# Performance work log

Measured on AMD Instinct MI355X. Metric: run time of the kernel, lower is better.

## Reference

```python
import jax, jax.numpy as jnp
import numpy as np

N = 20000      # nodes per snapshot
E = 160000     # edges per snapshot
T = 8          # timesteps
F_IN = 256     # nfeat
HEADS = 4      # GAT heads
C = 128        # nhid_graph (per-head GAT out, concat=False -> mean)
GH = 128       # nhid_gru
NC = 2         # nclass
NEG_SLOPE = 0.2


def setup_inputs() -> dict:
    key = jax.random.key(0)
    ks = jax.random.split(key, 16)
    s = 0.05
    return {
        "graph": jax.random.randint(ks[0], (T, 2, E), 0, N),
        "fts": jax.random.normal(ks[1], (T, N, F_IN), dtype=jnp.float32),
        "time_steps": T,
        # GATConv params (PyG-style): lin weight, att_src/att_dst, bias
        "W_gat": jax.random.normal(ks[2], (F_IN, HEADS * C), dtype=jnp.float32) * s,
        "att_src": jax.random.normal(ks[3], (HEADS, C), dtype=jnp.float32) * s,
        "att_dst": jax.random.normal(ks[4], (HEADS, C), dtype=jnp.float32) * s,
        "b_gat": jax.random.normal(ks[5], (C,), dtype=jnp.float32) * s,
        # GRU params (torch layout: [3H, in], gates order r,z,n)
        "W_ih": jax.random.normal(ks[6], (3 * GH, C), dtype=jnp.float32) * s,
        "W_hh": jax.random.normal(ks[7], (3 * GH, GH), dtype=jnp.float32) * s,
        "b_ih": jax.random.normal(ks[8], (3 * GH,), dtype=jnp.float32) * s,
        "b_hh": jax.random.normal(ks[9], (3 * GH,), dtype=jnp.float32) * s,
        # Attention ('general'): linear_in [H,H] no bias, linear_out [H,2H] no bias
        "W_att_in": jax.random.normal(ks[10], (GH, GH), dtype=jnp.float32) * s,
        "W_att_out": jax.random.normal(ks[11], (GH, 2 * GH), dtype=jnp.float32) * s,
        # final classifier
        "W_cls": jax.random.normal(ks[12], (NC, GH), dtype=jnp.float32) * s,
        "b_cls": jax.random.normal(ks[13], (NC,), dtype=jnp.float32) * s,
    }


def _segment_softmax(logits, seg, num_segments):
    # logits: [E', H], seg: [E'] destination node ids
    m = jax.ops.segment_max(logits, seg, num_segments=num_segments)
    m = jnp.where(jnp.isfinite(m), m, 0.0)
    e = jnp.exp(logits - m[seg])
    s = jax.ops.segment_sum(e, seg, num_segments=num_segments)
    return e / (s[seg] + 1e-16)


def _gat_step(x, edge_index, W_gat, att_src, att_dst, b_gat):
    # PyG GATConv: concat=False (mean over heads), negative_slope=0.2,
    # add_self_loops=True; eval mode so attention dropout is identity.
    n = x.shape[0]
    xw = (x @ W_gat).reshape(n, HEADS, C)                 # [N,H,C]
    loops = jnp.arange(n, dtype=edge_index.dtype)
    src = jnp.concatenate([edge_index[0], loops])         # [E']
    dst = jnp.concatenate([edge_index[1], loops])
    a_src = jnp.einsum('nhc,hc->nh', xw, att_src)         # [N,H]
    a_dst = jnp.einsum('nhc,hc->nh', xw, att_dst)
    alpha = jax.nn.leaky_relu(a_src[src] + a_dst[dst], NEG_SLOPE)  # [E',H]
    alpha = _segment_softmax(alpha, dst, n)
    msg = xw[src] * alpha[..., None]                      # [E',H,C]
    out = jax.ops.segment_sum(msg, dst, num_segments=n)   # [N,H,C]
    return out.mean(axis=1) + b_gat                       # [N,C]


def _gru(y, W_ih, W_hh, b_ih, b_hh):
    # y: [T, N, C]; torch GRU equations, h0 = 0
    n = y.shape[1]
    def step(h, x):
        gi = x @ W_ih.T + b_ih
        gh = h @ W_hh.T + b_hh
        i_r, i_z, i_n = jnp.split(gi, 3, axis=-1)
        h_r, h_z, h_n = jnp.split(gh, 3, axis=-1)
        r = jax.nn.sigmoid(i_r + h_r)
        z = jax.nn.sigmoid(i_z + h_z)
        nn_ = jnp.tanh(i_n + r * h_n)
        h_new = (1.0 - z) * nn_ + z * h
        return h_new, h_new
    h0 = jnp.zeros((n, GH), dtype=y.dtype)
    last, full = jax.lax.scan(step, h0, y)
    return full, last  # [T,N,GH], [N,GH]


def reference(graph, fts, time_steps, W_gat, att_src, att_dst, b_gat,
              W_ih, W_hh, b_ih, b_hh, W_att_in, W_att_out, W_cls, b_cls):
    # per-timestep GAT + leaky_relu(0.2)
    ys = [jax.nn.leaky_relu(
            _gat_step(fts[i], graph[i], W_gat, att_src, att_dst, b_gat),
            NEG_SLOPE)
          for i in range(time_steps)]
    y = jnp.stack(ys)                                     # [T,N,C]
    context, last = _gru(y, W_ih, W_hh, b_ih, b_hh)
    query = last[:, None, :]                              # [N,1,GH]
    context = jnp.transpose(context, (1, 0, 2))           # [N,T,GH]
    # Attention('general')
    q = query @ W_att_in.T                                # [N,1,GH]
    scores = jnp.einsum('nod,ntd->not', q, context)       # [N,1,T]
    w = jax.nn.softmax(scores, axis=-1)
    mix = jnp.einsum('not,ntd->nod', w, context)          # [N,1,GH]
    combined = jnp.concatenate([mix, q], axis=-1)         # [N,1,2GH]
    att_out = jnp.tanh(combined @ W_att_out.T)            # [N,1,GH]
    output = jax.nn.leaky_relu(att_out.reshape(-1, GH), NEG_SLOPE)
    logits = output @ W_cls.T + b_cls                     # [N,NC]
    return jax.nn.log_softmax(logits, axis=1)
```

## Files before the change

kernel.cpp:

```cpp
#include <hip/hip_runtime.h>
#include <hip/hip_bf16.h>
#include <math.h>

#define N_NODES 20000
#define N_EDGES 160000
#define T_STEPS 8
#define F_INC   256
#define HEADS   4
#define CCH     128
#define KC      512
#define GHD     128
#define G3      384
#define SLOPE   0.2f
#define SEG     (N_EDGES + N_NODES)

typedef unsigned short u16;
typedef __attribute__((ext_vector_type(8))) short bf16x8;
typedef __attribute__((ext_vector_type(4))) float f32x4;

__device__ __forceinline__ float leakyf(float x) { return x > 0.f ? x : SLOPE * x; }
__device__ __forceinline__ float b2f(u16 u) {
  union { unsigned int i; float f; } x; x.i = ((unsigned int)u) << 16; return x.f;
}
__device__ __forceinline__ u16 f2b(float f) {
  union { float f; unsigned int i; } u; u.f = f;
  unsigned int r = u.i + 0x7FFFu + ((u.i >> 16) & 1u);
  return (u16)(r >> 16);
}
__device__ __forceinline__ float sigf(float x) { return 1.f / (1.f + expf(-x)); }

__device__ __forceinline__ void gload16(const void* g, void* l) {
  __builtin_amdgcn_global_load_lds(
      (const __attribute__((address_space(1))) unsigned int*)g,
      (__attribute__((address_space(3))) unsigned int*)l, 16, 0, 0);
}

template <int OBF, int FUSE>
__global__ __launch_bounds__(256) void gemm_bf16(
    const u16* __restrict__ A, const u16* __restrict__ B,
    const float* __restrict__ bias, void* __restrict__ Cout,
    int M, int K, int Nt, int swz,
    const float* __restrict__ attS, const float* __restrict__ attD,
    float* __restrict__ asrc, float* __restrict__ adst)
{
  __shared__ u16 As[128][32];
  __shared__ u16 Bs[128][32];
  __shared__ float s_as[128], s_ad[128];
  const int tid  = threadIdx.x;
  const int wave = tid >> 6, lane = tid & 63;
  const int wr = (wave >> 1) * 64, wc = (wave & 1) * 64;
  int bx = blockIdx.x, by = blockIdx.y;
  if (swz) {
    const int gx = gridDim.x;
    const int nwg = gx * (int)gridDim.y;
    const int lin = by * gx + bx;
    const int q = nwg >> 3, r = nwg & 7;
    const int xcd = lin & 7, idx = lin >> 3;
    const int wg = (xcd < r ? xcd * (q + 1) : r * (q + 1) + (xcd - r) * q) + idx;
    bx = wg % gx; by = wg / gx;
  }
  const int bm = by * 128, bn = bx * 128;
  const int l15 = lane & 15, g = lane >> 4;

  if (FUSE && tid < 128) { s_as[tid] = 0.f; s_ad[tid] = 0.f; }

  const int sr = tid >> 2, sd = tid & 3;
  const int ss = sd ^ ((sr >> 1) & 3);
  const u16* aS0 = A + (size_t)min(bm + sr,      M - 1) * K + ss * 8;
  const u16* aS1 = A + (size_t)min(bm + 64 + sr, M - 1) * K + ss * 8;
  const u16* bS0 = B + (size_t)(bn + sr)      * K + ss * 8;
  const u16* bS1 = B + (size_t)(bn + 64 + sr) * K + ss * 8;
  u16* lA0 = &As[0][0] + (size_t)(tid & ~63) * 8;
  u16* lA1 = lA0 + 2048;
  u16* lB0 = &Bs[0][0] + (size_t)(tid & ~63) * 8;
  u16* lB1 = lB0 + 2048;

  f32x4 acc[4][4];
  #pragma unroll
  for (int m = 0; m < 4; ++m)
    #pragma unroll
    for (int n = 0; n < 4; ++n)
      #pragma unroll
      for (int j = 0; j < 4; ++j) acc[m][n][j] = 0.f;

  const int nK = K >> 5;
  for (int kt = 0; kt < nK; ++kt) {
    const int ko = kt * 32;
    gload16(aS0 + ko, lA0);
    gload16(aS1 + ko, lA1);
    gload16(bS0 + ko, lB0);
    gload16(bS1 + ko, lB1);
    __syncthreads();
    bf16x8 af[4], bfr[4];
    #pragma unroll
    for (int m = 0; m < 4; ++m) {
      int row = wr + m * 16 + l15;
      af[m] = *(const bf16x8*)&As[row][(g ^ ((row >> 1) & 3)) * 8];
      int rowb = wc + m * 16 + l15;
      bfr[m] = *(const bf16x8*)&Bs[rowb][(g ^ ((rowb >> 1) & 3)) * 8];
    }
    #pragma unroll
    for (int m = 0; m < 4; ++m)
      #pragma unroll
      for (int n = 0; n < 4; ++n)
        acc[m][n] = __builtin_amdgcn_mfma_f32_16x16x32_bf16(af[m], bfr[n], acc[m][n], 0, 0, 0);
    __syncthreads();
  }
  #pragma unroll
  for (int m = 0; m < 4; ++m) {
    int row0 = bm + wr + m * 16 + g * 4;
    #pragma unroll
    for (int n = 0; n < 4; ++n) {
      int col = bn + wc + n * 16 + l15;
      float bv = bias ? bias[col] : 0.f;
      #pragma unroll
      for (int j = 0; j < 4; ++j) {
        int row = row0 + j;
        if (row < M) {
          float v = acc[m][n][j] + bv;
          if (OBF) ((u16*)Cout)[(size_t)row * Nt + col] = f2b(v);
          else     ((float*)Cout)[(size_t)row * Nt + col] = v;
        }
      }
    }
  }
  if (FUSE) {
    float ps[4][4], pd[4][4];
    #pragma unroll
    for (int m = 0; m < 4; ++m)
      #pragma unroll
      for (int j = 0; j < 4; ++j) { ps[m][j] = 0.f; pd[m][j] = 0.f; }
    #pragma unroll
    for (int n = 0; n < 4; ++n) {
      int cl = wc + n * 16 + l15;
      float wsv = attS[bn + cl], wdv = attD[bn + cl];
      #pragma unroll
      for (int m = 0; m < 4; ++m)
        #pragma unroll
        for (int j = 0; j < 4; ++j) {
          ps[m][j] = fmaf(acc[m][n][j], wsv, ps[m][j]);
          pd[m][j] = fmaf(acc[m][n][j], wdv, pd[m][j]);
        }
    }
    #pragma unroll
    for (int m = 0; m < 4; ++m)
      #pragma unroll
      for (int j = 0; j < 4; ++j)
        #pragma unroll
        for (int msk = 8; msk >= 1; msk >>= 1) {
          ps[m][j] += __shfl_xor(ps[m][j], msk);
          pd[m][j] += __shfl_xor(pd[m][j], msk);
        }
    if (l15 == 0) {
      #pragma unroll
      for (int m = 0; m < 4; ++m)
        #pragma unroll
        for (int j = 0; j < 4; ++j) {
          atomicAdd(&s_as[wr + m * 16 + g * 4 + j], ps[m][j]);
          atomicAdd(&s_ad[wr + m * 16 + g * 4 + j], pd[m][j]);
        }
    }
    __syncthreads();
    if (tid < 128) {
      int row = bm + tid;
      if (row < M) {
        int h = bn >> 7;
        asrc[(size_t)row * 4 + h] = s_as[tid];
        adst[(size_t)row * 4 + h] = s_ad[tid];
      }
    }
  }
}

__global__ void convert_f32_bf16(const float* __restrict__ src, u16* __restrict__ dst, int n) {
  int i = (blockIdx.x * 256 + threadIdx.x) * 8;
  if (i >= n) return;
  float4 v0 = *(const float4*)(src + i);
  float4 v1 = *(const float4*)(src + i + 4);
  bf16x8 o;
  o[0] = (short)f2b(v0.x); o[1] = (short)f2b(v0.y);
  o[2] = (short)f2b(v0.z); o[3] = (short)f2b(v0.w);
  o[4] = (short)f2b(v1.x); o[5] = (short)f2b(v1.y);
  o[6] = (short)f2b(v1.z); o[7] = (short)f2b(v1.w);
  *(bf16x8*)(dst + i) = o;
}

__global__ void convert_weights(const float* __restrict__ w_ih, const float* __restrict__ w_hh,
                                const float* __restrict__ w_in, const float* __restrict__ w_out,
                                u16* __restrict__ wihb, u16* __restrict__ whhb,
                                u16* __restrict__ winb, u16* __restrict__ woutb)
{
  int i = blockIdx.x * 256 + threadIdx.x;
  const float* src; u16* dst; int base;
  if      (i < 6144)  { src = w_ih;  dst = wihb;  base = i; }
  else if (i < 12288) { src = w_hh;  dst = whhb;  base = i - 6144; }
  else if (i < 14336) { src = w_in;  dst = winb;  base = i - 12288; }
  else                { src = w_out; dst = woutb; base = i - 14336; }
  int o = base * 8;
  float4 v0 = *(const float4*)(src + o);
  float4 v1 = *(const float4*)(src + o + 4);
  bf16x8 ov;
  ov[0] = (short)f2b(v0.x); ov[1] = (short)f2b(v0.y);
  ov[2] = (short)f2b(v0.z); ov[3] = (short)f2b(v0.w);
  ov[4] = (short)f2b(v1.x); ov[5] = (short)f2b(v1.y);
  ov[6] = (short)f2b(v1.z); ov[7] = (short)f2b(v1.w);
  *(bf16x8*)(dst + o) = ov;
}

__global__ void conv_transpose_wgat(const float* __restrict__ src, u16* __restrict__ dst) {
  int idx = blockIdx.x * 256 + threadIdx.x;
  if (idx >= KC * F_INC) return;
  int n = idx >> 8, k = idx & 255;
  dst[(size_t)n * F_INC + k] = f2b(src[(size_t)k * KC + n]);
}

__global__ void count_kernel(const int* __restrict__ graph, int* __restrict__ counts) {
  int e = blockIdx.x * 256 + threadIdx.x;
  int t = blockIdx.y;
  if (e < N_EDGES) {
    int d = graph[(size_t)t * 2 * N_EDGES + N_EDGES + e];
    atomicAdd(&counts[t * N_NODES + d], 1);
  }
}

__global__ __launch_bounds__(1024) void scan_kernel(
    const int* __restrict__ counts, int* __restrict__ offs)
{
  const int t = blockIdx.x;
  const int tid = threadIdx.x, lane = tid & 63, w = tid >> 6;
  __shared__ int s_wt[16];
  int carry = 0;
  const int base_abs = t * SEG;
  for (int base = 0; base < N_NODES; base += 1024) {
    int i = base + tid;
    int v = (i < N_NODES) ? (counts[t * N_NODES + i] + 1) : 0;
    int x = v;
    #pragma unroll
    for (int d = 1; d < 64; d <<= 1) {
      int nvl = __shfl_up(x, d, 64);
      if (lane >= d) x += nvl;
    }
    if (lane == 63) s_wt[w] = x;
    __syncthreads();
    if (tid < 16) {
      int y = s_wt[tid];
      #pragma unroll
      for (int d = 1; d < 16; d <<= 1) {
        int nvl = __shfl_up(y, d, 64);
        if (tid >= d) y += nvl;
      }
      s_wt[tid] = y;
    }
    __syncthreads();
    int wbase = (w > 0) ? s_wt[w - 1] : 0;
    int total = s_wt[15];
    if (i < N_NODES) offs[t * (N_NODES + 1) + i] = base_abs + carry + wbase + x - v;
    carry += total;
    __syncthreads();
  }
  if (tid == 0) offs[t * (N_NODES + 1) + N_NODES] = base_abs + carry;
}

__global__ void scatter_kernel(const int* __restrict__ graph, const int* __restrict__ offs,
                               int* __restrict__ cursor, int* __restrict__ ssrc)
{
  int i = blockIdx.x * 256 + threadIdx.x;
  int t = blockIdx.y;
  if (i >= SEG) return;
  int s, d;
  if (i < N_EDGES) {
    s = graph[(size_t)t * 2 * N_EDGES + i];
    d = graph[(size_t)t * 2 * N_EDGES + N_EDGES + i];
  } else {
    s = d = i - N_EDGES;
  }
  int pos = offs[t * (N_NODES + 1) + d] + atomicAdd(&cursor[t * N_NODES + d], 1);
  ssrc[pos] = s;
}

__global__ __launch_bounds__(256) void aggregate_kernel(
    const u16* __restrict__ xw, const float* __restrict__ a_src,
    const float* __restrict__ a_dst, const float* __restrict__ b_gat,
    const int* __restrict__ offs, const int* __restrict__ ssrc,
    u16* __restrict__ yout)
{
  const int wv = threadIdx.x >> 6, lane = threadIdx.x & 63;
  const int nd = blockIdx.x * 4 + wv;
  const int t  = blockIdx.y;
  const int ob = t * (N_NODES + 1) + nd;
  const int beg = offs[ob], end = offs[ob + 1];
  const size_t rowbase = (size_t)t * N_NODES;
  const int he   = lane & 3;
  const int eidx = lane >> 2;
  const int hl   = lane >> 4;
  const float advh = a_dst[(rowbase + nd) * 4 + he];

  float m = -INFINITY, ssum = 0.f;
  float acc[8] = {0.f,0.f,0.f,0.f,0.f,0.f,0.f,0.f};

#define FMA8(W, X)                                                        \
    { float _w = (W);                                                     \
      acc[0] = fmaf(_w, __uint_as_float((unsigned)(X).x << 16), acc[0]);  \
      acc[1] = fmaf(_w, __uint_as_float((unsigned)(X).x & 0xffff0000u), acc[1]); \
      acc[2] = fmaf(_w, __uint_as_float((unsigned)(X).y << 16), acc[2]);  \
      acc[3] = fmaf(_w, __uint_as_float((unsigned)(X).y & 0xffff0000u), acc[3]); \
      acc[4] = fmaf(_w, __uint_as_float((unsigned)(X).z << 16), acc[4]);  \
      acc[5] = fmaf(_w, __uint_as_float((unsigned)(X).z & 0xffff0000u), acc[5]); \
      acc[6] = fmaf(_w, __uint_as_float((unsigned)(X).w << 16), acc[6]);  \
      acc[7] = fmaf(_w, __uint_as_float((unsigned)(X).w & 0xffff0000u), acc[7]); }
#define LDE(SVAR) (*(const int4*)&xw[(rowbase + (SVAR)) * KC + lane * 8])

  for (int base = beg; base < end; base += 16) {
    const int cnt = min(16, end - base);
    const int e = base + eidx;
    const int sidx = (e < end) ? ssrc[e] : ssrc[base];
    const float av = a_src[(rowbase + sidx) * 4 + he];
    const float a = (eidx < cnt) ? leakyf(av + advh) : -INFINITY;
    float cm = a;
    cm = fmaxf(cm, __shfl_xor(cm, 4));
    cm = fmaxf(cm, __shfl_xor(cm, 8));
    cm = fmaxf(cm, __shfl_xor(cm, 16));
    cm = fmaxf(cm, __shfl_xor(cm, 32));
    const float nm = fmaxf(m, cm);
    const float sc = expf(m - nm);
    const float w = expf(a - nm);
    float ts = w;
    ts += __shfl_xor(ts, 4);
    ts += __shfl_xor(ts, 8);
    ts += __shfl_xor(ts, 16);
    ts += __shfl_xor(ts, 32);
    ssum = ssum * sc + ts;
    m = nm;
    const float schl = __shfl(sc, hl);
    #pragma unroll
    for (int k = 0; k < 8; ++k) acc[k] *= schl;

    const int cpad = (cnt + 3) & ~3;
    int b4 = 0;
    for (; b4 + 8 <= cpad; b4 += 8) {
      const int s0 = __shfl(sidx, (b4 + 0) << 2);
      const int s1 = __shfl(sidx, (b4 + 1) << 2);
      const int s2 = __shfl(sidx, (b4 + 2) << 2);
      const int s3 = __shfl(sidx, (b4 + 3) << 2);
      const int s4 = __shfl(sidx, (b4 + 4) << 2);
      const int s5 = __shfl(sidx, (b4 + 5) << 2);
      const int s6 = __shfl(sidx, (b4 + 6) << 2);
      const int s7 = __shfl(sidx, (b4 + 7) << 2);
      const int4 x0 = LDE(s0); const int4 x1 = LDE(s1);
      const int4 x2 = LDE(s2); const int4 x3 = LDE(s3);
      const int4 x4 = LDE(s4); const int4 x5 = LDE(s5);
      const int4 x6 = LDE(s6); const int4 x7 = LDE(s7);
      const float w0 = __shfl(w, ((b4 + 0) << 2) + hl);
      const float w1 = __shfl(w, ((b4 + 1) << 2) + hl);
      const float w2 = __shfl(w, ((b4 + 2) << 2) + hl);
      const float w3 = __shfl(w, ((b4 + 3) << 2) + hl);
      const float w4 = __shfl(w, ((b4 + 4) << 2) + hl);
      const float w5 = __shfl(w, ((b4 + 5) << 2) + hl);
      const float w6 = __shfl(w, ((b4 + 6) << 2) + hl);
      const float w7 = __shfl(w, ((b4 + 7) << 2) + hl);
      FMA8(w0, x0); FMA8(w1, x1); FMA8(w2, x2); FMA8(w3, x3);
      FMA8(w4, x4); FMA8(w5, x5); FMA8(w6, x6); FMA8(w7, x7);
    }
    if (b4 < cpad) {
      const int s0 = __shfl(sidx, (b4 + 0) << 2);
      const int s1 = __shfl(sidx, (b4 + 1) << 2);
      const int s2 = __shfl(sidx, (b4 + 2) << 2);
      const int s3 = __shfl(sidx, (b4 + 3) << 2);
      const int4 x0 = LDE(s0); const int4 x1 = LDE(s1);
      const int4 x2 = LDE(s2); const int4 x3 = LDE(s3);
      const float w0 = __shfl(w, ((b4 + 0) << 2) + hl);
      const float w1 = __shfl(w, ((b4 + 1) << 2) + hl);
      const float w2 = __shfl(w, ((b4 + 2) << 2) + hl);
      const float w3 = __shfl(w, ((b4 + 3) << 2) + hl);
      FMA8(w0, x0); FMA8(w1, x1); FMA8(w2, x2); FMA8(w3, x3);
    }
  }
#undef LDE
#undef FMA8

  const float sh = __shfl(ssum, hl);
  const float inv = 1.f / (sh + 1e-16f);
  #pragma unroll
  for (int k = 0; k < 8; ++k) {
    acc[k] *= inv;
    acc[k] += __shfl_xor(acc[k], 16);
    acc[k] += __shfl_xor(acc[k], 32);
  }
  if (lane < 16) {
    bf16x8 ov;
    #pragma unroll
    for (int k = 0; k < 8; ++k) {
      float v = acc[k] * 0.25f + b_gat[lane * 8 + k];
      ov[k] = (short)f2b(leakyf(v));
    }
    *(bf16x8*)&yout[(rowbase + nd) * GHD + lane * 8] = ov;
  }
}

__global__ void gru_combine0(const u16* __restrict__ gi_t, const float* __restrict__ b_hh,
                             u16* __restrict__ ctx0, float* __restrict__ hf)
{
  int idx = blockIdx.x * 256 + threadIdx.x;
  if (idx >= N_NODES * GHD) return;
  int n = idx >> 7, c = idx & 127;
  size_t gb = (size_t)n * G3;
  float ir = b2f(gi_t[gb + c]), iz = b2f(gi_t[gb + 128 + c]), in_ = b2f(gi_t[gb + 256 + c]);
  float r = sigf(ir + b_hh[c]);
  float z = sigf(iz + b_hh[128 + c]);
  float nn = tanhf(in_ + r * b_hh[256 + c]);
  float h = (1.f - z) * nn;
  ctx0[idx] = f2b(h);
  hf[idx] = h;
}

__global__ __launch_bounds__(256) void gru_fused(
    const u16* __restrict__ hprev, const u16* __restrict__ Whh,
    const float* __restrict__ b_hh, const u16* __restrict__ gi_t,
    float* __restrict__ hf, u16* __restrict__ ctx_out)
{
  __shared__ u16 lds[64 * 384];
  u16 (*As)[32] = (u16(*)[32])lds;
  u16 (*Bs)[32] = (u16(*)[32])(lds + 64 * 32);
  const int tid = threadIdx.x, lane = tid & 63, wv = tid >> 6;
  const int l15 = lane & 15, g = lane >> 4;
  const int bm = blockIdx.x * 64;

  const int sr = tid >> 2, sd = tid & 3;
  const int ss = sd ^ ((sr >> 1) & 3);
  const u16* aS = hprev + (size_t)min(bm + sr, N_NODES - 1) * GHD + ss * 8;
  u16* lA = lds + (size_t)(tid & ~63) * 8;
  const u16* bS[6]; u16* lB[6];
  #pragma unroll
  for (int p = 0; p < 6; ++p) {
    int r = sr + p * 64;
    bS[p] = Whh + (size_t)r * GHD + ss * 8;
    lB[p] = lds + 64 * 32 + (size_t)(p * 256 + (tid & ~63)) * 8;
  }

  f32x4 acc[4][6];
  #pragma unroll
  for (int m = 0; m < 4; ++m)
    #pragma unroll
    for (int n = 0; n < 6; ++n)
      #pragma unroll
      for (int j = 0; j < 4; ++j) acc[m][n][j] = 0.f;

  #pragma unroll
  for (int kt = 0; kt < 4; ++kt) {
    const int ko = kt * 32;
    gload16(aS + ko, lA);
    #pragma unroll
    for (int p = 0; p < 6; ++p) gload16(bS[p] + ko, lB[p]);
    __syncthreads();
    bf16x8 af[4], bfr[6];
    #pragma unroll
    for (int m = 0; m < 4; ++m) {
      int row = m * 16 + l15;
      af[m] = *(const bf16x8*)&As[row][(g ^ ((row >> 1) & 3)) * 8];
    }
    #pragma unroll
    for (int n = 0; n < 6; ++n) {
      int row = wv * 96 + n * 16 + l15;
      bfr[n] = *(const bf16x8*)&Bs[row][(g ^ ((row >> 1) & 3)) * 8];
    }
    #pragma unroll
    for (int m = 0; m < 4; ++m)
      #pragma unroll
      for (int n = 0; n < 6; ++n)
        acc[m][n] = __builtin_amdgcn_mfma_f32_16x16x32_bf16(af[m], bfr[n], acc[m][n], 0, 0, 0);
    __syncthreads();
  }
  #pragma unroll
  for (int m = 0; m < 4; ++m)
    #pragma unroll
    for (int n = 0; n < 6; ++n) {
      int c = wv * 96 + n * 16 + l15;
      float bb = b_hh[c];
      #pragma unroll
      for (int j = 0; j < 4; ++j) {
        int r = m * 16 + g * 4 + j;
        lds[r * 384 + (((c >> 3) ^ (r & 7)) << 3) + (c & 7)] = f2b(acc[m][n][j] + bb);
      }
    }
  __syncthreads();
  {
    int r = tid >> 2, gr = bm + r;
    if (gr < N_NODES) {
      const int cg = (tid & 3) * 32;
      const size_t gb = (size_t)gr * G3;
      const size_t cb = (size_t)gr * GHD;
      #pragma unroll
      for (int q = 0; q < 4; ++q) {
        int c0 = cg + q * 8;
        int sl0 = ((c0 >> 3) ^ (r & 7));
        int sl1 = (((128 + c0) >> 3) ^ (r & 7));
        int sl2 = (((256 + c0) >> 3) ^ (r & 7));
        bf16x8 hr8 = *(bf16x8*)&lds[r * 384 + sl0 * 8];
        bf16x8 hz8 = *(bf16x8*)&lds[r * 384 + sl1 * 8];
        bf16x8 hn8 = *(bf16x8*)&lds[r * 384 + sl2 * 8];
        bf16x8 ir8 = *(const bf16x8*)&gi_t[gb + c0];
        bf16x8 iz8 = *(const bf16x8*)&gi_t[gb + 128 + c0];
        bf16x8 in8 = *(const bf16x8*)&gi_t[gb + 256 + c0];
        float4 hp0 = *(const float4*)&hf[cb + c0];
        float4 hp1 = *(const float4*)&hf[cb + c0 + 4];
        float hp[8] = {hp0.x, hp0.y, hp0.z, hp0.w, hp1.x, hp1.y, hp1.z, hp1.w};
        float cv[8];
        bf16x8 hv;
        #pragma unroll
        for (int k = 0; k < 8; ++k) {
          float rr = sigf(b2f((u16)ir8[k]) + b2f((u16)hr8[k]));
          float zz = sigf(b2f((u16)iz8[k]) + b2f((u16)hz8[k]));
          float nn = tanhf(b2f((u16)in8[k]) + rr * b2f((u16)hn8[k]));
          float h = (1.f - zz) * nn + zz * hp[k];
          cv[k] = h;
          hv[k] = (short)f2b(h);
        }
        *(float4*)&hf[cb + c0]     = make_float4(cv[0], cv[1], cv[2], cv[3]);
        *(float4*)&hf[cb + c0 + 4] = make_float4(cv[4], cv[5], cv[6], cv[7]);
        *(bf16x8*)&ctx_out[cb + c0] = hv;
      }
    }
  }
}

__global__ __launch_bounds__(256) void attn_mid(
    const u16* __restrict__ ctx, const float* __restrict__ q,
    u16* __restrict__ comb)
{
  const int node = blockIdx.x * 4 + (threadIdx.x >> 6);
  const int lane = threadIdx.x & 63;
  if (node >= N_NODES) return;
  const float q0 = q[(size_t)node * GHD + lane];
  const float q1 = q[(size_t)node * GHD + 64 + lane];
  float c0[T_STEPS], c1[T_STEPS], w[T_STEPS];
  float mx = -1e30f;
  #pragma unroll
  for (int t = 0; t < T_STEPS; ++t) {
    const u16* cr = ctx + ((size_t)t * N_NODES + node) * GHD;
    c0[t] = b2f(cr[lane]); c1[t] = b2f(cr[64 + lane]);
    float p = q0 * c0[t] + q1 * c1[t];
    #pragma unroll
    for (int m = 32; m >= 1; m >>= 1) p += __shfl_xor(p, m);
    w[t] = p;
    mx = fmaxf(mx, p);
  }
  float s = 0.f;
  #pragma unroll
  for (int t = 0; t < T_STEPS; ++t) { w[t] = expf(w[t] - mx); s += w[t]; }
  const float inv = 1.f / s;
  float m0 = 0.f, m1 = 0.f;
  #pragma unroll
  for (int t = 0; t < T_STEPS; ++t) { m0 = fmaf(w[t], c0[t], m0); m1 = fmaf(w[t], c1[t], m1); }
  m0 *= inv; m1 *= inv;
  u16* cb = comb + (size_t)node * 2 * GHD;
  cb[lane]       = f2b(m0);
  cb[64 + lane]  = f2b(m1);
  cb[128 + lane] = f2b(q0);
  cb[192 + lane] = f2b(q1);
}

__global__ __launch_bounds__(256) void logits_kernel(
    const u16* __restrict__ ao, const float* __restrict__ W_cls,
    const float* __restrict__ b_cls, float* __restrict__ out)
{
  const int node = blockIdx.x * 4 + (threadIdx.x >> 6);
  const int lane = threadIdx.x & 63;
  if (node >= N_NODES) return;
  float o0 = leakyf(tanhf(b2f(ao[(size_t)node * GHD + lane])));
  float o1 = leakyf(tanhf(b2f(ao[(size_t)node * GHD + 64 + lane])));
  float p0 = o0 * W_cls[lane] + o1 * W_cls[64 + lane];
  float p1 = o0 * W_cls[128 + lane] + o1 * W_cls[192 + lane];
  #pragma unroll
  for (int m = 32; m >= 1; m >>= 1) { p0 += __shfl_xor(p0, m); p1 += __shfl_xor(p1, m); }
  if (lane == 0) {
    float l0 = p0 + b_cls[0];
    float l1 = p1 + b_cls[1];
    float mx = fmaxf(l0, l1);
    float lse = mx + logf(expf(l0 - mx) + expf(l1 - mx));
    out[(size_t)node * 2 + 0] = l0 - lse;
    out[(size_t)node * 2 + 1] = l1 - lse;
  }
}

extern "C" void kernel_launch(void* const* d_in, const int* in_sizes, int n_in,
                              void* d_out, int out_size, void* d_ws, size_t ws_size,
                              hipStream_t stream)
{
  const int*   graph     = (const int*)  d_in[0];
  const float* fts       = (const float*)d_in[1];
  const float* W_gat     = (const float*)d_in[3];
  const float* att_src   = (const float*)d_in[4];
  const float* att_dst   = (const float*)d_in[5];
  const float* b_gat     = (const float*)d_in[6];
  const float* W_ih      = (const float*)d_in[7];
  const float* W_hh      = (const float*)d_in[8];
  const float* b_ih      = (const float*)d_in[9];
  const float* b_hh      = (const float*)d_in[10];
  const float* W_att_in  = (const float*)d_in[11];
  const float* W_att_out = (const float*)d_in[12];
  const float* W_cls     = (const float*)d_in[13];
  const float* b_cls     = (const float*)d_in[14];
  float* out = (float*)d_out;

  char* ws = (char*)d_ws;
  size_t off = 0;
  auto alloc = [&](size_t bytes) {
    void* p = ws + off;
    off = (off + bytes + 255) & ~(size_t)255;
    return p;
  };
  const size_t NT = (size_t)T_STEPS * N_NODES;
  u16*   wgatT = (u16*)alloc((size_t)KC * F_INC * 2);
  u16*   wihb  = (u16*)alloc((size_t)G3 * GHD * 2);
  u16*   whhb  = (u16*)alloc((size_t)G3 * GHD * 2);
  u16*   winb  = (u16*)alloc((size_t)GHD * GHD * 2);
  u16*   woutb = (u16*)alloc((size_t)GHD * 2 * GHD * 2);
  u16*   fbf   = (u16*)alloc(NT * F_INC * 2);
  u16*   xw    = (u16*)alloc(NT * KC * 2);
  float* asrc  = (float*)alloc(NT * 4 * 4);
  float* adst  = (float*)alloc(NT * 4 * 4);
  u16*   yall  = (u16*)alloc(NT * GHD * 2);
  u16*   giall = (u16*)alloc(NT * G3 * 2);
  u16*   ctx   = (u16*)alloc(NT * GHD * 2);
  float* hf    = (float*)alloc((size_t)N_NODES * GHD * 4);
  float* qf    = (float*)alloc((size_t)N_NODES * GHD * 4);
  u16*   comb  = (u16*)alloc((size_t)N_NODES * 2 * GHD * 2);
  u16*   aob   = (u16*)alloc((size_t)N_NODES * GHD * 2);
  int* counts  = (int*)alloc((size_t)2 * T_STEPS * N_NODES * 4);
  int* cursor  = counts + T_STEPS * N_NODES;
  int* offs    = (int*)alloc((size_t)T_STEPS * (N_NODES + 1) * 4);
  int* ssrc    = (int*)alloc((size_t)T_STEPS * SEG * 4);

  conv_transpose_wgat<<<dim3((KC * F_INC + 255) / 256), 256, 0, stream>>>(W_gat, wgatT);
  convert_weights<<<dim3(72), 256, 0, stream>>>(W_ih, W_hh, W_att_in, W_att_out,
                                                wihb, whhb, winb, woutb);

  hipMemsetAsync(counts, 0, (size_t)2 * T_STEPS * N_NODES * 4, stream);
  count_kernel<<<dim3(N_EDGES / 256, T_STEPS), 256, 0, stream>>>(graph, counts);
  scan_kernel<<<dim3(T_STEPS), 1024, 0, stream>>>(counts, offs);
  scatter_kernel<<<dim3((SEG + 255) / 256, T_STEPS), 256, 0, stream>>>(graph, offs, cursor, ssrc);

  convert_f32_bf16<<<dim3((int)(NT * F_INC / 8 / 256)), 256, 0, stream>>>(
      fts, fbf, (int)(NT * F_INC));

  gemm_bf16<1, 1><<<dim3(KC / 128, (int)(NT / 128)), 256, 0, stream>>>(
      fbf, wgatT, nullptr, xw, (int)NT, F_INC, KC, 1, att_src, att_dst, asrc, adst);

  aggregate_kernel<<<dim3(N_NODES / 4, T_STEPS), 256, 0, stream>>>(
      xw, asrc, adst, b_gat, offs, ssrc, yall);

  gemm_bf16<1, 0><<<dim3(G3 / 128, (int)(NT / 128)), 256, 0, stream>>>(
      yall, wihb, b_ih, giall, (int)NT, GHD, G3, 1, nullptr, nullptr, nullptr, nullptr);

  gru_combine0<<<dim3(N_NODES * GHD / 256), 256, 0, stream>>>(giall, b_hh, ctx, hf);
  for (int t = 1; t < T_STEPS; ++t) {
    gru_fused<<<dim3((N_NODES + 63) / 64), 256, 0, stream>>>(
        ctx + (size_t)(t - 1) * N_NODES * GHD, whhb, b_hh,
        giall + (size_t)t * N_NODES * G3, hf,
        ctx + (size_t)t * N_NODES * GHD);
  }

  gemm_bf16<0, 0><<<dim3(1, (N_NODES + 127) / 128), 256, 0, stream>>>(
      ctx + (size_t)(T_STEPS - 1) * N_NODES * GHD, winb, nullptr, qf,
      N_NODES, GHD, GHD, 0, nullptr, nullptr, nullptr, nullptr);
  attn_mid<<<dim3(N_NODES / 4), 256, 0, stream>>>(ctx, qf, comb);
  gemm_bf16<1, 0><<<dim3(1, (N_NODES + 127) / 128), 256, 0, stream>>>(
      comb, woutb, nullptr, aob, N_NODES, 2 * GHD, GHD, 0, nullptr, nullptr, nullptr, nullptr);
  logits_kernel<<<dim3(N_NODES / 4), 256, 0, stream>>>(aob, W_cls, b_cls, out);
}
```

Measured before the change: 827.0 us.

## Fuse fp32->bf16 conversion into GAT GEMM and persist GRU across timesteps

The GAT projection GEMM now loads fp32 features straight into LDS and converts them to bf16 with packed convert instructions, so the separate conversion kernel and its bf16 feature buffer go away. The seven per-timestep GRU launches plus the initial combine kernel become one kernel. Each block owns 32 nodes and keeps the hidden state in LDS and registers across all timesteps, which removes the hf fp32 round trips and the repeated hprev reloads. In exchange the A tile in LDS doubles in size, W_hh is reloaded from global memory every step, and the GRU grid uses smaller 32-row tiles.

New measurement: 744.4 us. -10.0%, faster.

```diff
diff --git a/kernel.cpp b/kernel.cpp
--- a/kernel.cpp
+++ b/kernel.cpp
@@ -35,17 +35,28 @@
       (__attribute__((address_space(3))) unsigned int*)l, 16, 0, 0);
 }
 
-template <int OBF, int FUSE>
+__device__ __forceinline__ bf16x8 cvt8(f32x4 lo, f32x4 hi) {
+  union { unsigned int u[4]; bf16x8 v; } r;
+  asm("v_cvt_pk_bf16_f32 %0, %1, %2" : "=v"(r.u[0]) : "v"(lo[0]), "v"(lo[1]));
+  asm("v_cvt_pk_bf16_f32 %0, %1, %2" : "=v"(r.u[1]) : "v"(lo[2]), "v"(lo[3]));
+  asm("v_cvt_pk_bf16_f32 %0, %1, %2" : "=v"(r.u[2]) : "v"(hi[0]), "v"(hi[1]));
+  asm("v_cvt_pk_bf16_f32 %0, %1, %2" : "=v"(r.u[3]) : "v"(hi[2]), "v"(hi[3]));
+  return r.v;
+}
+
+template <int OBF, int FUSE, int AFP32>
 __global__ __launch_bounds__(256) void gemm_bf16(
-    const u16* __restrict__ A, const u16* __restrict__ B,
+    const void* __restrict__ Ain, const u16* __restrict__ B,
     const float* __restrict__ bias, void* __restrict__ Cout,
     int M, int K, int Nt, int swz,
     const float* __restrict__ attS, const float* __restrict__ attD,
     float* __restrict__ asrc, float* __restrict__ adst)
 {
-  __shared__ u16 As[128][32];
+  __shared__ __align__(16) char AsRaw[128 * 32 * 4];
   __shared__ u16 Bs[128][32];
   __shared__ float s_as[128], s_ad[128];
+  float* AsF = (float*)AsRaw;
+  u16 (*Asb)[32] = (u16(*)[32])AsRaw;
   const int tid  = threadIdx.x;
   const int wave = tid >> 6, lane = tid & 63;
   const int wr = (wave >> 1) * 64, wc = (wave & 1) * 64;
@@ -66,12 +77,27 @@
 
   const int sr = tid >> 2, sd = tid & 3;
   const int ss = sd ^ ((sr >> 1) & 3);
-  const u16* aS0 = A + (size_t)min(bm + sr,      M - 1) * K + ss * 8;
-  const u16* aS1 = A + (size_t)min(bm + 64 + sr, M - 1) * K + ss * 8;
+  const u16* aS0 = 0; const u16* aS1 = 0; u16* lA0 = 0; u16* lA1 = 0;
+  const float* aF[4]; float* lAF[4];
+  if (AFP32) {
+    const float* Af = (const float*)Ain;
+    const int row0 = tid >> 3, sd8 = tid & 7;
+    const int ss8 = sd8 ^ (row0 & 7);
+    #pragma unroll
+    for (int p = 0; p < 4; ++p) {
+      int row = row0 + p * 32;
+      aF[p] = Af + (size_t)min(bm + row, M - 1) * K + ss8 * 4;
+      lAF[p] = AsF + (size_t)(p * 256 + (tid & ~63)) * 4;
+    }
+  } else {
+    const u16* Ab = (const u16*)Ain;
+    aS0 = Ab + (size_t)min(bm + sr,      M - 1) * K + ss * 8;
+    aS1 = Ab + (size_t)min(bm + 64 + sr, M - 1) * K + ss * 8;
+    lA0 = (u16*)AsRaw + (size_t)(tid & ~63) * 8;
+    lA1 = lA0 + 2048;
+  }
   const u16* bS0 = B + (size_t)(bn + sr)      * K + ss * 8;
   const u16* bS1 = B + (size_t)(bn + 64 + sr) * K + ss * 8;
-  u16* lA0 = &As[0][0] + (size_t)(tid & ~63) * 8;
-  u16* lA1 = lA0 + 2048;
   u16* lB0 = &Bs[0][0] + (size_t)(tid & ~63) * 8;
   u16* lB1 = lB0 + 2048;
 
@@ -86,8 +112,13 @@
   const int nK = K >> 5;
   for (int kt = 0; kt < nK; ++kt) {
     const int ko = kt * 32;
-    gload16(aS0 + ko, lA0);
-    gload16(aS1 + ko, lA1);
+    if (AFP32) {
+      #pragma unroll
+      for (int p = 0; p < 4; ++p) gload16(aF[p] + ko, lAF[p]);
+    } else {
+      gload16(aS0 + ko, lA0);
+      gload16(aS1 + ko, lA1);
+    }
     gload16(bS0 + ko, lB0);
     gload16(bS1 + ko, lB1);
     __syncthreads();
@@ -95,7 +126,14 @@
     #pragma unroll
     for (int m = 0; m < 4; ++m) {
       int row = wr + m * 16 + l15;
-      af[m] = *(const bf16x8*)&As[row][(g ^ ((row >> 1) & 3)) * 8];
+      if (AFP32) {
+        int s0 = (2 * g) ^ (row & 7), s1 = (2 * g + 1) ^ (row & 7);
+        f32x4 lo = *(const f32x4*)&AsF[row * 32 + s0 * 4];
+        f32x4 hi = *(const f32x4*)&AsF[row * 32 + s1 * 4];
+        af[m] = cvt8(lo, hi);
+      } else {
+        af[m] = *(const bf16x8*)&Asb[row][(g ^ ((row >> 1) & 3)) * 8];
+      }
       int rowb = wc + m * 16 + l15;
       bfr[m] = *(const bf16x8*)&Bs[rowb][(g ^ ((rowb >> 1) & 3)) * 8];
     }
@@ -170,19 +208,6 @@
       }
     }
   }
-}
-
-__global__ void convert_f32_bf16(const float* __restrict__ src, u16* __restrict__ dst, int n) {
-  int i = (blockIdx.x * 256 + threadIdx.x) * 8;
-  if (i >= n) return;
-  float4 v0 = *(const float4*)(src + i);
-  float4 v1 = *(const float4*)(src + i + 4);
-  bf16x8 o;
-  o[0] = (short)f2b(v0.x); o[1] = (short)f2b(v0.y);
-  o[2] = (short)f2b(v0.z); o[3] = (short)f2b(v0.w);
-  o[4] = (short)f2b(v1.x); o[5] = (short)f2b(v1.y);
-  o[6] = (short)f2b(v1.z); o[7] = (short)f2b(v1.w);
-  *(bf16x8*)(dst + i) = o;
 }
 
 __global__ void convert_weights(const float* __restrict__ w_ih, const float* __restrict__ w_hh,
@@ -397,129 +422,139 @@
   }
 }
 
-__global__ void gru_combine0(const u16* __restrict__ gi_t, const float* __restrict__ b_hh,
-                             u16* __restrict__ ctx0, float* __restrict__ hf)
-{
-  int idx = blockIdx.x * 256 + threadIdx.x;
-  if (idx >= N_NODES * GHD) return;
-  int n = idx >> 7, c = idx & 127;
-  size_t gb = (size_t)n * G3;
-  float ir = b2f(gi_t[gb + c]), iz = b2f(gi_t[gb + 128 + c]), in_ = b2f(gi_t[gb + 256 + c]);
-  float r = sigf(ir + b_hh[c]);
-  float z = sigf(iz + b_hh[128 + c]);
-  float nn = tanhf(in_ + r * b_hh[256 + c]);
-  float h = (1.f - z) * nn;
-  ctx0[idx] = f2b(h);
-  hf[idx] = h;
-}
-
-__global__ __launch_bounds__(256) void gru_fused(
-    const u16* __restrict__ hprev, const u16* __restrict__ Whh,
-    const float* __restrict__ b_hh, const u16* __restrict__ gi_t,
-    float* __restrict__ hf, u16* __restrict__ ctx_out)
-{
-  __shared__ u16 lds[64 * 384];
-  u16 (*As)[32] = (u16(*)[32])lds;
-  u16 (*Bs)[32] = (u16(*)[32])(lds + 64 * 32);
+__global__ __launch_bounds__(256) void gru_seq(
+    const u16* __restrict__ Whh, const float* __restrict__ b_hh,
+    const u16* __restrict__ giall, u16* __restrict__ ctx)
+{
+  __shared__ u16 hA[32][128];
+  __shared__ u16 reg2[12288];
+  u16 (*Bs)[32] = (u16(*)[32])reg2;
   const int tid = threadIdx.x, lane = tid & 63, wv = tid >> 6;
   const int l15 = lane & 15, g = lane >> 4;
-  const int bm = blockIdx.x * 64;
+  const int bm = blockIdx.x * 32;
 
   const int sr = tid >> 2, sd = tid & 3;
-  const int ss = sd ^ ((sr >> 1) & 3);
-  const u16* aS = hprev + (size_t)min(bm + sr, N_NODES - 1) * GHD + ss * 8;
-  u16* lA = lds + (size_t)(tid & ~63) * 8;
+  const int ssb = sd ^ ((sr >> 1) & 3);
   const u16* bS[6]; u16* lB[6];
   #pragma unroll
   for (int p = 0; p < 6; ++p) {
-    int r = sr + p * 64;
-    bS[p] = Whh + (size_t)r * GHD + ss * 8;
-    lB[p] = lds + 64 * 32 + (size_t)(p * 256 + (tid & ~63)) * 8;
-  }
-
-  f32x4 acc[4][6];
-  #pragma unroll
-  for (int m = 0; m < 4; ++m)
-    #pragma unroll
-    for (int n = 0; n < 6; ++n)
-      #pragma unroll
-      for (int j = 0; j < 4; ++j) acc[m][n][j] = 0.f;
-
-  #pragma unroll
-  for (int kt = 0; kt < 4; ++kt) {
-    const int ko = kt * 32;
-    gload16(aS + ko, lA);
-    #pragma unroll
-    for (int p = 0; p < 6; ++p) gload16(bS[p] + ko, lB[p]);
-    __syncthreads();
-    bf16x8 af[4], bfr[6];
-    #pragma unroll
-    for (int m = 0; m < 4; ++m) {
-      int row = m * 16 + l15;
-      af[m] = *(const bf16x8*)&As[row][(g ^ ((row >> 1) & 3)) * 8];
-    }
-    #pragma unroll
-    for (int n = 0; n < 6; ++n) {
-      int row = wv * 96 + n * 16 + l15;
-      bfr[n] = *(const bf16x8*)&Bs[row][(g ^ ((row >> 1) & 3)) * 8];
-    }
-    #pragma unroll
-    for (int m = 0; m < 4; ++m)
+    bS[p] = Whh + (size_t)(sr + p * 64) * GHD + ssb * 8;
+    lB[p] = reg2 + (size_t)(p * 256 + (tid & ~63)) * 8;
+  }
+  float bbv[6];
+  #pragma unroll
+  for (int n = 0; n < 6; ++n) bbv[n] = b_hh[wv * 96 + n * 16 + l15];
+
+  const int cr = tid >> 3;
+  const int cg = (tid & 7) * 8;
+  const int grow = bm + cr;
+  const size_t gb = (size_t)grow * G3;
+  const size_t cb = (size_t)grow * GHD;
+  float hp[2][8];
+
+  #pragma unroll
+  for (int q = 0; q < 2; ++q) {
+    const int c0 = cg + q * 64;
+    bf16x8 ir8 = *(const bf16x8*)&giall[gb + c0];
+    bf16x8 iz8 = *(const bf16x8*)&giall[gb + 128 + c0];
+    bf16x8 in8 = *(const bf16x8*)&giall[gb + 256 + c0];
+    float4 br0 = *(const float4*)&b_hh[c0];       float4 br1 = *(const float4*)&b_hh[c0 + 4];
+    float4 bz0 = *(const float4*)&b_hh[128 + c0]; float4 bz1 = *(const float4*)&b_hh[128 + c0 + 4];
+    float4 bn0 = *(const float4*)&b_hh[256 + c0]; float4 bn1 = *(const float4*)&b_hh[256 + c0 + 4];
+    float bhr[8] = {br0.x, br0.y, br0.z, br0.w, br1.x, br1.y, br1.z, br1.w};
+    float bhz[8] = {bz0.x, bz0.y, bz0.z, bz0.w, bz1.x, bz1.y, bz1.z, bz1.w};
+    float bhn[8] = {bn0.x, bn0.y, bn0.z, bn0.w, bn1.x, bn1.y, bn1.z, bn1.w};
+    bf16x8 hv;
+    #pragma unroll
+    for (int k = 0; k < 8; ++k) {
+      float rr = sigf(b2f((u16)ir8[k]) + bhr[k]);
+      float zz = sigf(b2f((u16)iz8[k]) + bhz[k]);
+      float nn = tanhf(b2f((u16)in8[k]) + rr * bhn[k]);
+      float h = (1.f - zz) * nn;
+      hp[q][k] = h;
+      hv[k] = (short)f2b(h);
+    }
+    const int sl = (c0 >> 3) ^ (cr & 7);
+    *(bf16x8*)&hA[cr][sl * 8] = hv;
+    *(bf16x8*)&ctx[cb + c0] = hv;
+  }
+  __syncthreads();
+
+  for (int t = 1; t < T_STEPS; ++t) {
+    const u16* gi_t = giall + (size_t)t * N_NODES * G3;
+    u16* ctx_t = ctx + (size_t)t * N_NODES * GHD;
+    f32x4 acc[2][6];
+    #pragma unroll
+    for (int m = 0; m < 2; ++m)
       #pragma unroll
       for (int n = 0; n < 6; ++n)
-        acc[m][n] = __builtin_amdgcn_mfma_f32_16x16x32_bf16(af[m], bfr[n], acc[m][n], 0, 0, 0);
-    __syncthreads();
-  }
-  #pragma unroll
-  for (int m = 0; m < 4; ++m)
-    #pragma unroll
-    for (int n = 0; n < 6; ++n) {
-      int c = wv * 96 + n * 16 + l15;
-      float bb = b_hh[c];
-      #pragma unroll
-      for (int j = 0; j < 4; ++j) {
-        int r = m * 16 + g * 4 + j;
-        lds[r * 384 + (((c >> 3) ^ (r & 7)) << 3) + (c & 7)] = f2b(acc[m][n][j] + bb);
-      }
-    }
-  __syncthreads();
-  {
-    int r = tid >> 2, gr = bm + r;
-    if (gr < N_NODES) {
-      const int cg = (tid & 3) * 32;
-      const size_t gb = (size_t)gr * G3;
-      const size_t cb = (size_t)gr * GHD;
-      #pragma unroll
-      for (int q = 0; q < 4; ++q) {
-        int c0 = cg + q * 8;
-        int sl0 = ((c0 >> 3) ^ (r & 7));
-        int sl1 = (((128 + c0) >> 3) ^ (r & 7));
-        int sl2 = (((256 + c0) >> 3) ^ (r & 7));
-        bf16x8 hr8 = *(bf16x8*)&lds[r * 384 + sl0 * 8];
-        bf16x8 hz8 = *(bf16x8*)&lds[r * 384 + sl1 * 8];
-        bf16x8 hn8 = *(bf16x8*)&lds[r * 384 + sl2 * 8];
-        bf16x8 ir8 = *(const bf16x8*)&gi_t[gb + c0];
-        bf16x8 iz8 = *(const bf16x8*)&gi_t[gb + 128 + c0];
-        bf16x8 in8 = *(const bf16x8*)&gi_t[gb + 256 + c0];
-        float4 hp0 = *(const float4*)&hf[cb + c0];
-        float4 hp1 = *(const float4*)&hf[cb + c0 + 4];
-        float hp[8] = {hp0.x, hp0.y, hp0.z, hp0.w, hp1.x, hp1.y, hp1.z, hp1.w};
-        float cv[8];
-        bf16x8 hv;
         #pragma unroll
-        for (int k = 0; k < 8; ++k) {
-          float rr = sigf(b2f((u16)ir8[k]) + b2f((u16)hr8[k]));
-          float zz = sigf(b2f((u16)iz8[k]) + b2f((u16)hz8[k]));
-          float nn = tanhf(b2f((u16)in8[k]) + rr * b2f((u16)hn8[k]));
-          float h = (1.f - zz) * nn + zz * hp[k];
-          cv[k] = h;
-          hv[k] = (short)f2b(h);
+        for (int j = 0; j < 4; ++j) acc[m][n][j] = 0.f;
+
+    #pragma unroll
+    for (int kt = 0; kt < 4; ++kt) {
+      const int ko = kt * 32;
+      #pragma unroll
+      for (int p = 0; p < 6; ++p) gload16(bS[p] + ko, lB[p]);
+      __syncthreads();
+      bf16x8 af[2], bfr[6];
+      #pragma unroll
+      for (int m = 0; m < 2; ++m) {
+        int row = m * 16 + l15;
+        int sl = (kt * 4 + g) ^ (row & 7);
+        af[m] = *(const bf16x8*)&hA[row][sl * 8];
+      }
+      #pragma unroll
+      for (int n = 0; n < 6; ++n) {
+        int rowb = wv * 96 + n * 16 + l15;
+        bfr[n] = *(const bf16x8*)&Bs[rowb][(g ^ ((rowb >> 1) & 3)) * 8];
+      }
+      #pragma unroll
+      for (int m = 0; m < 2; ++m)
+        #pragma unroll
+        for (int n = 0; n < 6; ++n)
+          acc[m][n] = __builtin_amdgcn_mfma_f32_16x16x32_bf16(af[m], bfr[n], acc[m][n], 0, 0, 0);
+      __syncthreads();
+    }
+    #pragma unroll
+    for (int m = 0; m < 2; ++m)
+      #pragma unroll
+      for (int n = 0; n < 6; ++n) {
+        int c = wv * 96 + n * 16 + l15;
+        #pragma unroll
+        for (int j = 0; j < 4; ++j) {
+          int r = m * 16 + g * 4 + j;
+          reg2[r * 384 + (((c >> 3) ^ (r & 7)) << 3) + (c & 7)] = f2b(acc[m][n][j] + bbv[n]);
         }
-        *(float4*)&hf[cb + c0]     = make_float4(cv[0], cv[1], cv[2], cv[3]);
-        *(float4*)&hf[cb + c0 + 4] = make_float4(cv[4], cv[5], cv[6], cv[7]);
-        *(bf16x8*)&ctx_out[cb + c0] = hv;
-      }
-    }
+      }
+    __syncthreads();
+    #pragma unroll
+    for (int q = 0; q < 2; ++q) {
+      const int c0 = cg + q * 64;
+      const int sl0 = ((c0 >> 3) ^ (cr & 7));
+      const int sl1 = (((128 + c0) >> 3) ^ (cr & 7));
+      const int sl2 = (((256 + c0) >> 3) ^ (cr & 7));
+      bf16x8 hr8 = *(bf16x8*)&reg2[cr * 384 + sl0 * 8];
+      bf16x8 hz8 = *(bf16x8*)&reg2[cr * 384 + sl1 * 8];
+      bf16x8 hn8 = *(bf16x8*)&reg2[cr * 384 + sl2 * 8];
+      bf16x8 ir8 = *(const bf16x8*)&gi_t[gb + c0];
+      bf16x8 iz8 = *(const bf16x8*)&gi_t[gb + 128 + c0];
+      bf16x8 in8 = *(const bf16x8*)&gi_t[gb + 256 + c0];
+      bf16x8 hv;
+      #pragma unroll
+      for (int k = 0; k < 8; ++k) {
+        float rr = sigf(b2f((u16)ir8[k]) + b2f((u16)hr8[k]));
+        float zz = sigf(b2f((u16)iz8[k]) + b2f((u16)hz8[k]));
+        float nn = tanhf(b2f((u16)in8[k]) + rr * b2f((u16)hn8[k]));
+        float h = (1.f - zz) * nn + zz * hp[q][k];
+        hp[q][k] = h;
+        hv[k] = (short)f2b(h);
+      }
+      const int slh = (c0 >> 3) ^ (cr & 7);
+      *(bf16x8*)&hA[cr][slh * 8] = hv;
+      *(bf16x8*)&ctx_t[cb + c0] = hv;
+    }
+    __syncthreads();
   }
 }
 
@@ -615,14 +650,12 @@
   u16*   whhb  = (u16*)alloc((size_t)G3 * GHD * 2);
   u16*   winb  = (u16*)alloc((size_t)GHD * GHD * 2);
   u16*   woutb = (u16*)alloc((size_t)GHD * 2 * GHD * 2);
-  u16*   fbf   = (u16*)alloc(NT * F_INC * 2);
   u16*   xw    = (u16*)alloc(NT * KC * 2);
   float* asrc  = (float*)alloc(NT * 4 * 4);
   float* adst  = (float*)alloc(NT * 4 * 4);
   u16*   yall  = (u16*)alloc(NT * GHD * 2);
   u16*   giall = (u16*)alloc(NT * G3 * 2);
   u16*   ctx   = (u16*)alloc(NT * GHD * 2);
-  float* hf    = (float*)alloc((size_t)N_NODES * GHD * 4);
   float* qf    = (float*)alloc((size_t)N_NODES * GHD * 4);
   u16*   comb  = (u16*)alloc((size_t)N_NODES * 2 * GHD * 2);
   u16*   aob   = (u16*)alloc((size_t)N_NODES * GHD * 2);
@@ -640,31 +673,22 @@
   scan_kernel<<<dim3(T_STEPS), 1024, 0, stream>>>(counts, offs);
   scatter_kernel<<<dim3((SEG + 255) / 256, T_STEPS), 256, 0, stream>>>(graph, offs, cursor, ssrc);
 
-  convert_f32_bf16<<<dim3((int)(NT * F_INC / 8 / 256)), 256, 0, stream>>>(
-      fts, fbf, (int)(NT * F_INC));
-
-  gemm_bf16<1, 1><<<dim3(KC / 128, (int)(NT / 128)), 256, 0, stream>>>(
-      fbf, wgatT, nullptr, xw, (int)NT, F_INC, KC, 1, att_src, att_dst, asrc, adst);
+  gemm_bf16<1, 1, 1><<<dim3(KC / 128, (int)(NT / 128)), 256, 0, stream>>>(
+      fts, wgatT, nullptr, xw, (int)NT, F_INC, KC, 1, att_src, att_dst, asrc, adst);
 
   aggregate_kernel<<<dim3(N_NODES / 4, T_STEPS), 256, 0, stream>>>(
       xw, asrc, adst, b_gat, offs, ssrc, yall);
 
-  gemm_bf16<1, 0><<<dim3(G3 / 128, (int)(NT / 128)), 256, 0, stream>>>(
+  gemm_bf16<1, 0, 0><<<dim3(G3 / 128, (int)(NT / 128)), 256, 0, stream>>>(
       yall, wihb, b_ih, giall, (int)NT, GHD, G3, 1, nullptr, nullptr, nullptr, nullptr);
 
-  gru_combine0<<<dim3(N_NODES * GHD / 256), 256, 0, stream>>>(giall, b_hh, ctx, hf);
-  for (int t = 1; t < T_STEPS; ++t) {
-    gru_fused<<<dim3((N_NODES + 63) / 64), 256, 0, stream>>>(
-        ctx + (size_t)(t - 1) * N_NODES * GHD, whhb, b_hh,
-        giall + (size_t)t * N_NODES * G3, hf,
-        ctx + (size_t)t * N_NODES * GHD);
-  }
-
-  gemm_bf16<0, 0><<<dim3(1, (N_NODES + 127) / 128), 256, 0, stream>>>(
+  gru_seq<<<dim3(N_NODES / 32), 256, 0, stream>>>(whhb, b_hh, giall, ctx);
+
+  gemm_bf16<0, 0, 0><<<dim3(1, (N_NODES + 127) / 128), 256, 0, stream>>>(
       ctx + (size_t)(T_STEPS - 1) * N_NODES * GHD, winb, nullptr, qf,
       N_NODES, GHD, GHD, 0, nullptr, nullptr, nullptr, nullptr);
   attn_mid<<<dim3(N_NODES / 4), 256, 0, stream>>>(ctx, qf, comb);
-  gemm_bf16<1, 0><<<dim3(1, (N_NODES + 127) / 128), 256, 0, stream>>>(
+  gemm_bf16<1, 0, 0><<<dim3(1, (N_NODES + 127) / 128), 256, 0, stream>>>(
       comb, woutb, nullptr, aob, N_NODES, 2 * GHD, GHD, 0, nullptr, nullptr, nullptr, nullptr);
   logits_kernel<<<dim3(N_NODES / 4), 256, 0, stream>>>(aob, W_cls, b_cls, out);
 }
```
